# Kernel optimization log

Measured on AMD Instinct MI355X. Metric: run time of the kernel, lower is better.

## Reference

```python
import jax, jax.numpy as jnp
import numpy as np

B, C, H, W = 256, 32, 64, 64


def _affine_grid(theta, Hs, Ws):
    # theta: [B,2,3]; align_corners=False (PyTorch default). Returns [B,H,W,2] with (x,y) order.
    xs = (2.0 * jnp.arange(Ws, dtype=theta.dtype) + 1.0) / Ws - 1.0  # [W]
    ys = (2.0 * jnp.arange(Hs, dtype=theta.dtype) + 1.0) / Hs - 1.0  # [H]
    Xg, Yg = jnp.meshgrid(xs, ys)                                    # [H,W] each
    base = jnp.stack([Xg, Yg, jnp.ones_like(Xg)], axis=-1)           # [H,W,3]
    return jnp.einsum('bij,hwj->bhwi', theta, base)                  # [B,H,W,2]


def _grid_sample_bilinear(x, grid):
    # x: [B,C,H,W]; grid: [B,H,W,2] normalized (x,y); bilinear, zero padding, align_corners=False.
    Bs, Cs, Hs, Ws = x.shape
    gx = (grid[..., 0] + 1.0) * (Ws * 0.5) - 0.5
    gy = (grid[..., 1] + 1.0) * (Hs * 0.5) - 0.5
    x0 = jnp.floor(gx); y0 = jnp.floor(gy)
    x1 = x0 + 1.0;      y1 = y0 + 1.0
    wx1 = gx - x0; wx0 = 1.0 - wx1
    wy1 = gy - y0; wy0 = 1.0 - wy1

    def corner(xf, yf, w):
        valid = (xf >= 0) & (xf <= Ws - 1) & (yf >= 0) & (yf <= Hs - 1)
        xi = jnp.clip(xf, 0, Ws - 1).astype(jnp.int32)
        yi = jnp.clip(yf, 0, Hs - 1).astype(jnp.int32)
        vals = jax.vmap(lambda img, yy, xx: img[:, yy, xx])(x, yi, xi)  # [B,C,H,W] gather
        return vals * (w * valid)[:, None, :, :]

    return (corner(x0, y0, wx0 * wy0) + corner(x1, y0, wx1 * wy0)
            + corner(x0, y1, wx0 * wy1) + corner(x1, y1, wx1 * wy1))


def reference(x, w1, b1, w2, b2, w3, b3):
    Bs = x.shape[0]
    xs = x.reshape(Bs, -1)
    xs = jax.nn.relu(xs @ w1.T + b1)
    xs = jax.nn.relu(xs @ w2.T + b2)
    theta = (xs @ w3.T + b3).reshape(Bs, 2, 3)
    grid = _affine_grid(theta, x.shape[2], x.shape[3])
    return _grid_sample_bilinear(x, grid)


def setup_inputs() -> dict:
    key = jax.random.key(0)
    ks = jax.random.split(key, 8)
    fan1 = C * H * W
    x = jax.random.normal(ks[0], (B, C, H, W), dtype=jnp.float32)
    w1 = jax.random.normal(ks[1], (32, fan1), dtype=jnp.float32) / np.sqrt(fan1)
    b1 = jax.random.normal(ks[2], (32,), dtype=jnp.float32) * 0.01
    w2 = jax.random.normal(ks[3], (32, 32), dtype=jnp.float32) / np.sqrt(32.0)
    b2 = jax.random.normal(ks[4], (32,), dtype=jnp.float32) * 0.01
    w3 = jax.random.normal(ks[5], (6, 32), dtype=jnp.float32) * 0.001
    identity = jnp.array([1.0, 0.0, 0.0, 0.0, 1.0, 0.0], dtype=jnp.float32)
    b3 = identity + jax.random.normal(ks[6], (6,), dtype=jnp.float32) * 0.01
    return {"x": x, "w1": w1, "b1": b1, "w2": w2, "b2": b2, "w3": w3, "b3": b3}
```

## Files before the change

kernel.cpp:

```cpp
#include <hip/hip_runtime.h>
#include <hip/hip_bf16.h>


#define K_TOT 131072
#define KC    256
#define PKN   1024
#define STRB  ((size_t)PKN * 32)

typedef short s16x8 __attribute__((ext_vector_type(8)));
typedef float f32x4 __attribute__((ext_vector_type(4)));

__device__ __forceinline__ short f2bf(float f) {
    return __builtin_bit_cast(short, __float2bfloat16(f));
}

__device__ __forceinline__ s16x8 cvt8(float4 a, float4 b) {
    s16x8 r;
    r[0] = f2bf(a.x); r[1] = f2bf(a.y); r[2] = f2bf(a.z); r[3] = f2bf(a.w);
    r[4] = f2bf(b.x); r[5] = f2bf(b.y); r[6] = f2bf(b.z); r[7] = f2bf(b.w);
    return r;
}

__device__ __forceinline__ void gload_lds16(const float* g, float* l) {
    __builtin_amdgcn_global_load_lds(
        (const __attribute__((address_space(1))) void*)(g),
        (__attribute__((address_space(3))) void*)(l),
        16, 0, 0);
}

__global__ __launch_bounds__(256) void st_p1k(const float* __restrict__ x,
                                              const float* __restrict__ w1,
                                              float* __restrict__ partial) {
    __shared__ __align__(16) char smem[49152];
    float* xbuf0 = (float*)smem;
    float* xbuf1 = (float*)(smem + 16384);
    s16x8* wlds  = (s16x8*)(smem + 32768);

    const int bid  = blockIdx.x;
    const int t    = threadIdx.x;
    const int wv   = t >> 6;
    const int lane = t & 63;
    const int m    = lane & 15;
    const int kb   = lane >> 4;
    const int jh   = wv & 1;
    const int kh   = wv >> 1;

    const int xcd  = bid & 7;
    const int q    = bid >> 3;
    const int kc   = xcd * 64 + (q >> 1);
    const int half = q & 1;
    const size_t k0 = (size_t)kc * KC;

    {
        const int b0 = half * 128;
#pragma unroll
        for (int i2 = 0; i2 < 4; ++i2) {
            const int r = wv * 4 + i2;
            const float* gsrc = x + (size_t)(b0 + r) * K_TOT + k0 + ((lane ^ (r & 7)) << 2);
            gload_lds16(gsrc, xbuf0 + r * 256);
        }
    }
#pragma unroll
    for (int i = 0; i < 4; ++i) {
        const int f  = i * 256 + t;
        const int fm = f & 15, fk = (f >> 4) & 3, fj = (f >> 6) & 1, fs = f >> 7;
        const float* wp = w1 + (size_t)(fj * 16 + fm) * K_TOT + k0 + fs * 32 + fk * 8;
        wlds[f] = cvt8(*(const float4*)wp, *(const float4*)(wp + 4));
    }

    const int pk = kc * 2 + kh;
    const int sw = m & 7;
#pragma unroll
    for (int it = 0; it < 8; ++it) {
        __syncthreads();

        if (it < 7) {
            float* nbuf = ((it + 1) & 1) ? xbuf1 : xbuf0;
            const int b0n = half * 128 + (it + 1) * 16;
#pragma unroll
            for (int i2 = 0; i2 < 4; ++i2) {
                const int r = wv * 4 + i2;
                const float* gsrc = x + (size_t)(b0n + r) * K_TOT + k0 + ((lane ^ (r & 7)) << 2);
                gload_lds16(gsrc, nbuf + r * 256);
            }
        }

        const float* cbuf = (it & 1) ? xbuf1 : xbuf0;
        const float* xr = cbuf + m * 256;
        f32x4 acc = {0.f, 0.f, 0.f, 0.f};
#pragma unroll
        for (int sss = 0; sss < 4; ++sss) {
            const int gb = kh * 32 + sss * 8 + kb * 2;
            const float4 fa = *(const float4*)(xr + ((gb ^ sw) << 2));
            const float4 fb = *(const float4*)(xr + (((gb + 1) ^ sw) << 2));
            const s16x8 af = cvt8(fa, fb);
            const s16x8 bf = wlds[((kh * 4 + sss) * 2 + jh) * 64 + lane];
            acc = __builtin_amdgcn_mfma_f32_16x16x32_bf16(af, bf, acc, 0, 0, 0);
        }
        const int b0 = half * 128 + it * 16;
        float* p0 = partial + (size_t)(b0 + kb * 4) * STRB + (size_t)pk * 32 + jh * 16 + m;
#pragma unroll
        for (int rr = 0; rr < 4; ++rr)
            p0[(size_t)rr * STRB] = acc[rr];
    }
}

__global__ __launch_bounds__(256) void st_p2k(const float* __restrict__ partial,
                                              const float* __restrict__ b1,
                                              const float* __restrict__ w2,
                                              const float* __restrict__ b2,
                                              const float* __restrict__ w3,
                                              const float* __restrict__ b3,
                                              float* __restrict__ theta) {
    const int b = blockIdx.x;
    const int t = threadIdx.x;
    const float* pb = partial + (size_t)b * STRB;

    float4 v = {0.f, 0.f, 0.f, 0.f};
#pragma unroll
    for (int i = 0; i < 32; ++i) {
        const float4 u = *(const float4*)(pb + (size_t)(i * 256 + t) * 4);
        v.x += u.x; v.y += u.y; v.z += u.z; v.w += u.w;
    }

    __shared__ float4 red[256];
    __shared__ float s1s[32];
    __shared__ float s2s[32];
    red[t] = v;
    __syncthreads();
#pragma unroll
    for (int off = 128; off >= 8; off >>= 1) {
        if (t < off) {
            float4 a = red[t];
            const float4 c = red[t + off];
            a.x += c.x; a.y += c.y; a.z += c.z; a.w += c.w;
            red[t] = a;
        }
        __syncthreads();
    }
    if (t < 8) {
        const float4 qd = red[t];
        s1s[4 * t + 0] = fmaxf(qd.x + b1[4 * t + 0], 0.f);
        s1s[4 * t + 1] = fmaxf(qd.y + b1[4 * t + 1], 0.f);
        s1s[4 * t + 2] = fmaxf(qd.z + b1[4 * t + 2], 0.f);
        s1s[4 * t + 3] = fmaxf(qd.w + b1[4 * t + 3], 0.f);
    }
    __syncthreads();
    if (t < 32) {
        float vv = b2[t];
#pragma unroll
        for (int i = 0; i < 32; ++i) vv += w2[t * 32 + i] * s1s[i];
        s2s[t] = fmaxf(vv, 0.f);
    }
    __syncthreads();
    if (t < 8) {
        float vv = 0.f;
        if (t < 6) {
            vv = b3[t];
#pragma unroll
            for (int i = 0; i < 32; ++i) vv += w3[t * 32 + i] * s2s[i];
        }
        theta[b * 8 + t] = vv;
    }
}

__global__ __launch_bounds__(256) void st_p3k(const float* __restrict__ x,
                                              const float* __restrict__ theta,
                                              float* __restrict__ out) {
    const int bid = blockIdx.x;
    const int b   = bid >> 3;
    const int h0  = (bid & 7) * 8;
    const int t   = threadIdx.x;
    const int w   = t & 63;
    const int c0  = t >> 6;

    const float* tb = theta + b * 8;
    const float t0 = tb[0], t1 = tb[1], t2 = tb[2];
    const float t3 = tb[3], t4 = tb[4], t5 = tb[5];

    for (int r = 0; r < 8; ++r) {
        const int h = h0 + r;
        const float xs = ((float)w - 31.5f) * 0.03125f;
        const float ys = ((float)h - 31.5f) * 0.03125f;
        const float gxn = fmaf(t1, ys, fmaf(t0, xs, t2));
        const float gyn = fmaf(t4, ys, fmaf(t3, xs, t5));
        const float gx = fmaf(gxn, 32.f, 31.5f);
        const float gy = fmaf(gyn, 32.f, 31.5f);
        const float x0f = floorf(gx), y0f = floorf(gy);
        const float wx1 = gx - x0f, wx0 = 1.f - wx1;
        const float wy1 = gy - y0f, wy0 = 1.f - wy1;
        const int ix = (int)x0f, iy = (int)y0f;
        const bool vx0 = (ix >= 0) && (ix < 64);
        const bool vx1 = (ix >= -1) && (ix < 63);
        const bool vy0 = (iy >= 0) && (iy < 64);
        const bool vy1 = (iy >= -1) && (iy < 63);
        const int cx0 = min(max(ix, 0), 63);
        const int cx1 = min(max(ix + 1, 0), 63);
        const int cy0 = min(max(iy, 0), 63);
        const int cy1 = min(max(iy + 1, 0), 63);
        const float w00 = wx0 * wy0 * ((vx0 && vy0) ? 1.f : 0.f);
        const float w10 = wx1 * wy0 * ((vx1 && vy0) ? 1.f : 0.f);
        const float w01 = wx0 * wy1 * ((vx0 && vy1) ? 1.f : 0.f);
        const float w11 = wx1 * wy1 * ((vx1 && vy1) ? 1.f : 0.f);
        const int r0 = cy0 * 64, r1 = cy1 * 64;
#pragma unroll
        for (int i = 0; i < 8; ++i) {
            const int c = c0 + 4 * i;
            const float* img = x + (((size_t)b * 32 + c) << 12);
            const float v = w00 * img[r0 + cx0] + w10 * img[r0 + cx1]
                          + w01 * img[r1 + cx0] + w11 * img[r1 + cx1];
            __builtin_nontemporal_store(v, &out[(((size_t)b * 32 + c) << 12) + h * 64 + w]);
        }
    }
}

extern "C" void kernel_launch(void* const* d_in, const int* in_sizes, int n_in,
                              void* d_out, int out_size, void* d_ws, size_t ws_size,
                              hipStream_t stream) {
    const float* x  = (const float*)d_in[0];
    const float* w1 = (const float*)d_in[1];
    const float* b1 = (const float*)d_in[2];
    const float* w2 = (const float*)d_in[3];
    const float* b2 = (const float*)d_in[4];
    const float* w3 = (const float*)d_in[5];
    const float* b3 = (const float*)d_in[6];
    float* out = (float*)d_out;
    float* ws  = (float*)d_ws;
    float* partial = ws;
    float* theta   = ws + (size_t)256 * STRB;

    st_p1k<<<1024, 256, 0, stream>>>(x, w1, partial);
    st_p2k<<<256, 256, 0, stream>>>(partial, b1, w2, b2, w3, b3, theta);
    st_p3k<<<2048, 256, 0, stream>>>(x, theta, out);
}
```

Baseline: 88.33 us.

## Triple-buffer x tiles with prefetch depth two, keep w1 fragments in registers

The first kernel now stages x through three LDS buffers and prefetches two batch tiles ahead. It replaces __syncthreads with explicit vmcnt waits plus a raw barrier so loads for the next tiles stay in flight while the current tile is computed. The w1 weights are loaded straight into registers per lane and converted to bf16 fragments, rather than being staged through LDS. This is meant to hide global-load latency and remove one LDS round-trip, at the cost of more registers and hand-counted waitcnt values that depend on the compiler's instruction order.

```diff
diff --git a/kernel.cpp b/kernel.cpp
--- a/kernel.cpp
+++ b/kernel.cpp
@@ -31,10 +31,7 @@
 __global__ __launch_bounds__(256) void st_p1k(const float* __restrict__ x,
                                               const float* __restrict__ w1,
                                               float* __restrict__ partial) {
-    __shared__ __align__(16) char smem[49152];
-    float* xbuf0 = (float*)smem;
-    float* xbuf1 = (float*)(smem + 16384);
-    s16x8* wlds  = (s16x8*)(smem + 32768);
+    __shared__ __align__(16) float xbuf[3][16 * KC];
 
     const int bid  = blockIdx.x;
     const int t    = threadIdx.x;
@@ -51,42 +48,52 @@
     const int half = q & 1;
     const size_t k0 = (size_t)kc * KC;
 
-    {
-        const int b0 = half * 128;
+    const float* wq = w1 + (size_t)(jh * 16 + m) * K_TOT + k0 + (size_t)kh * 128 + kb * 8;
+    float4 wr[8];
+#pragma unroll
+    for (int sss = 0; sss < 4; ++sss) {
+        wr[2 * sss]     = *(const float4*)(wq + sss * 32);
+        wr[2 * sss + 1] = *(const float4*)(wq + sss * 32 + 4);
+    }
+
+#pragma unroll
+    for (int pt = 0; pt < 2; ++pt) {
 #pragma unroll
         for (int i2 = 0; i2 < 4; ++i2) {
             const int r = wv * 4 + i2;
+            const int b0 = half * 128 + pt * 16;
             const float* gsrc = x + (size_t)(b0 + r) * K_TOT + k0 + ((lane ^ (r & 7)) << 2);
-            gload_lds16(gsrc, xbuf0 + r * 256);
-        }
-    }
-#pragma unroll
-    for (int i = 0; i < 4; ++i) {
-        const int f  = i * 256 + t;
-        const int fm = f & 15, fk = (f >> 4) & 3, fj = (f >> 6) & 1, fs = f >> 7;
-        const float* wp = w1 + (size_t)(fj * 16 + fm) * K_TOT + k0 + fs * 32 + fk * 8;
-        wlds[f] = cvt8(*(const float4*)wp, *(const float4*)(wp + 4));
-    }
+            gload_lds16(gsrc, &xbuf[pt][r * KC]);
+        }
+    }
+
+    s16x8 wf[4];
+#pragma unroll
+    for (int sss = 0; sss < 4; ++sss) wf[sss] = cvt8(wr[2 * sss], wr[2 * sss + 1]);
 
     const int pk = kc * 2 + kh;
     const int sw = m & 7;
+
 #pragma unroll
     for (int it = 0; it < 8; ++it) {
-        __syncthreads();
-
-        if (it < 7) {
-            float* nbuf = ((it + 1) & 1) ? xbuf1 : xbuf0;
-            const int b0n = half * 128 + (it + 1) * 16;
+        if (it == 0)              asm volatile("s_waitcnt vmcnt(4)"  ::: "memory");
+        else if (it == 1 || it == 7) asm volatile("s_waitcnt vmcnt(8)"  ::: "memory");
+        else                      asm volatile("s_waitcnt vmcnt(12)" ::: "memory");
+        __builtin_amdgcn_s_barrier();
+        __builtin_amdgcn_sched_barrier(0);
+
+        if (it + 2 < 8) {
+            float* nbuf = xbuf[(it + 2) % 3];
+            const int b0n = half * 128 + (it + 2) * 16;
 #pragma unroll
             for (int i2 = 0; i2 < 4; ++i2) {
                 const int r = wv * 4 + i2;
                 const float* gsrc = x + (size_t)(b0n + r) * K_TOT + k0 + ((lane ^ (r & 7)) << 2);
-                gload_lds16(gsrc, nbuf + r * 256);
+                gload_lds16(gsrc, nbuf + r * KC);
             }
         }
 
-        const float* cbuf = (it & 1) ? xbuf1 : xbuf0;
-        const float* xr = cbuf + m * 256;
+        const float* xr = &xbuf[it % 3][m * KC];
         f32x4 acc = {0.f, 0.f, 0.f, 0.f};
 #pragma unroll
         for (int sss = 0; sss < 4; ++sss) {
@@ -94,9 +101,9 @@
             const float4 fa = *(const float4*)(xr + ((gb ^ sw) << 2));
             const float4 fb = *(const float4*)(xr + (((gb + 1) ^ sw) << 2));
             const s16x8 af = cvt8(fa, fb);
-            const s16x8 bf = wlds[((kh * 4 + sss) * 2 + jh) * 64 + lane];
-            acc = __builtin_amdgcn_mfma_f32_16x16x32_bf16(af, bf, acc, 0, 0, 0);
-        }
+            acc = __builtin_amdgcn_mfma_f32_16x16x32_bf16(af, wf[sss], acc, 0, 0, 0);
+        }
+
         const int b0 = half * 128 + it * 16;
         float* p0 = partial + (size_t)(b0 + kb * 4) * STRB + (size_t)pk * 32 + jh * 16 + m;
 #pragma unroll
```

Result: no change. 87.88 us (-0.5%).
